# Performance work log

Hardware: AMD Instinct MI355X
Metric: run time of the kernel (lower is better)

## Reference

```python
import jax, jax.numpy as jnp
import numpy as np

FS = 20.832e6      # sampling rate [Hz]
FDEMOD = 5.208e6   # demodulation frequency [Hz]
C = 1540.0         # sound speed [m/s]
FNUM = 1.0
MIN_W = 1e-3
EPS = 1e-5         # BatchNorm eps
EVENT = 0
TWO_PI = 2.0 * np.pi


def _cba(x, w, b, g, beta, pad):
    # Conv2d (NCHW) + BatchNorm2d (training-mode batch stats, biased var) + ReLU
    y = jax.lax.conv_general_dilated(x, w, (1, 1), ((0, 0), (pad, pad)),
                                     dimension_numbers=('NCHW', 'OIHW', 'NCHW'))
    y = y + b[None, :, None, None]
    mu = jnp.mean(y, axis=(0, 2, 3), keepdims=True)
    var = jnp.mean((y - mu) ** 2, axis=(0, 2, 3), keepdims=True)
    y = (y - mu) * jax.lax.rsqrt(var + EPS) * g[None, :, None, None] + beta[None, :, None, None]
    return jax.nn.relu(y)


def _forward(idata, qdata, angles, ele_pos, time_zero, grid,
             conv_w1, conv_b1, bn_g1, bn_b1,
             conv_w2, conv_b2, bn_g2, bn_b2,
             conv_w3, conv_b3, bn_g3, bn_b3,
             conv_w4, conv_b4, bn_g4, bn_b4):
    # --- normalization of raw I/Q data ---
    nrm = jnp.max(jnp.sqrt(idata ** 2 + qdata ** 2))
    idat = idata / nrm
    qdat = qdata / nrm
    H, Wd = grid.shape[:2]
    pix = grid.reshape(-1, 3)                               # [P,3]
    E = ele_pos.shape[0]
    ns = idat.shape[-1]
    ang = angles[EVENT]
    # --- delays in samples: plane-wave tx delay + per-element rx focus delay ---
    txdel = (pix[:, 0] * jnp.sin(ang) + pix[:, 2] * jnp.cos(ang)
             + time_zero[EVENT] * C) * (FS / C)             # [P]
    rxdel = jnp.linalg.norm(pix[None, :, :] - ele_pos[:, None, :], axis=-1) * (FS / C)  # [E,P]
    delays = txdel[None, :] + rxdel                         # [E,P]
    # --- 1D linear interp with zero padding ---
    # (grid_sample(bilinear, align_corners=False) on a 1xN image with the
    #  coordinate mapping in the source is exactly sampling at `delays`)
    d0 = jnp.floor(delays)
    frac = delays - d0
    d0i = d0.astype(jnp.int32)

    def gather(sig, idx):  # sig [E,ns], idx [E,P]
        v = jnp.take_along_axis(sig, jnp.clip(idx, 0, ns - 1), axis=1)
        return jnp.where((idx >= 0) & (idx < ns), v, 0.0)

    isig, qsig = idat[EVENT], qdat[EVENT]                   # [E,ns]
    ifoc = gather(isig, d0i) * (1.0 - frac) + gather(isig, d0i + 1) * frac
    qfoc = gather(qsig, d0i) * (1.0 - frac) + gather(qsig, d0i + 1) * frac
    # --- complex demodulation rotation ---
    tshift = delays / FS - pix[None, :, 2] * 2.0 / C
    theta = TWO_PI * FDEMOD * tshift
    ct, st = jnp.cos(theta), jnp.sin(theta)
    ir = ifoc * ct - qfoc * st
    qr = qfoc * ct + ifoc * st
    # [1,H,W,E,2]  (== torch idas/qdas view + squeeze(-2))
    inputData = jnp.transpose(jnp.stack([ir, qr], axis=-1), (1, 0, 2)).reshape(H, Wd, E, 2)[None]
    # --- receive apodization (orthogonal f-number mask), [H,W,E] ---
    v = pix[None, :, :] - ele_pos[:, None, :]
    vx, vz = v[:, :, 0], v[:, :, 2]
    px = pix[None, :, 0]
    # |vz/vx| > fnum written division-free as |vz| > fnum*|vx| (equivalent since vz>0)
    mrx = ((jnp.abs(vz) > FNUM * jnp.abs(vx)) | (jnp.abs(vx) <= MIN_W)
           | ((vx >= MIN_W) & (px <= ele_pos[0, 0]))
           | ((vx <= -MIN_W) & (px >= ele_pos[-1, 0])))
    apod_rx = jnp.transpose(mrx.astype(jnp.float32).reshape(E, H, Wd), (1, 2, 0))
    # --- transmit apodization (plane-wave footprint), [H,W] ---
    x_proj = pix[:, 0] - pix[:, 2] * jnp.tan(ang)
    mtx = (x_proj >= ele_pos[0, 0] * 1.2) & (x_proj <= ele_pos[-1, 0] * 1.2)
    apod_tx = mtx.astype(jnp.float32).reshape(H, Wd)
    inputData = inputData * apod_rx[None, :, :, :, None] * apod_tx[None, :, :, None, None]
    # --- per-element weighting CNN over [1, 2, H*W, E] ---
    x = jnp.transpose(inputData, (0, 4, 3, 1, 2)).reshape(1, 2, E, H * Wd)
    x = jnp.swapaxes(x, 2, 3)                               # [1,2,HW,E]
    x = _cba(x, conv_w1, conv_b1, bn_g1, bn_b1, 32)
    x = _cba(x, conv_w2, conv_b2, bn_g2, bn_b2, 7)
    x = _cba(x, conv_w3, conv_b3, bn_g3, bn_b3, 7)
    x = _cba(x, conv_w4, conv_b4, bn_g4, bn_b4, 1)          # [1,1,HW,E]
    weights = jnp.swapaxes(x[:, 0], 1, 2).reshape(1, E, H, Wd)
    singleW = jnp.sum(weights, axis=1)                      # [1,H,W]
    comp = jnp.mean(inputData * singleW[:, :, :, None, None], axis=-2)  # [1,H,W,2]
    mag = jnp.sqrt(jnp.sum(comp ** 2, axis=-1))
    ydb = 20.0 * jnp.log10(mag + 1e-20)
    y = ydb[0]
    return y - jnp.max(y)


def setup_inputs():
    key = jax.random.key(0)
    ks = jax.random.split(key, 8)
    na, ne, ns = 16, 128, 2048
    H, Wd = 128, 256
    idata = jax.random.normal(ks[0], (na, ne, ns), jnp.float32)
    qdata = jax.random.normal(ks[1], (na, ne, ns), jnp.float32)
    angles = jnp.linspace(-0.1, 0.1, na, dtype=jnp.float32)
    ex = jnp.linspace(-19.05e-3, 19.05e-3, ne, dtype=jnp.float32)
    ele_pos = jnp.stack([ex, jnp.zeros(ne, jnp.float32), jnp.zeros(ne, jnp.float32)], axis=-1)
    time_zero = jnp.zeros((na,), jnp.float32)
    xg = jnp.linspace(-17e-3, 17e-3, H, dtype=jnp.float32)
    zg = jnp.linspace(5e-3, 55e-3, Wd, dtype=jnp.float32)
    gx, gz = jnp.meshgrid(xg, zg, indexing='ij')
    grid = jnp.stack([gx, jnp.zeros_like(gx), gz], axis=-1)

    def conv_init(k, o, i, kh, kw):
        return jax.random.normal(k, (o, i, kh, kw), jnp.float32) * (1.0 / np.sqrt(i * kh * kw))

    return dict(idata=idata, qdata=qdata, angles=angles, ele_pos=ele_pos,
                time_zero=time_zero, grid=grid,
                conv_w1=conv_init(ks[2], 8, 2, 1, 65), conv_b1=jnp.zeros(8, jnp.float32),
                bn_g1=jnp.ones(8, jnp.float32), bn_b1=jnp.zeros(8, jnp.float32),
                conv_w2=conv_init(ks[3], 8, 8, 1, 15), conv_b2=jnp.zeros(8, jnp.float32),
                bn_g2=jnp.ones(8, jnp.float32), bn_b2=jnp.zeros(8, jnp.float32),
                conv_w3=conv_init(ks[4], 8, 8, 1, 15), conv_b3=jnp.zeros(8, jnp.float32),
                bn_g3=jnp.ones(8, jnp.float32), bn_b3=jnp.zeros(8, jnp.float32),
                conv_w4=conv_init(ks[5], 1, 8, 1, 3), conv_b4=jnp.zeros(1, jnp.float32),
                bn_g4=jnp.ones(1, jnp.float32), bn_b4=jnp.zeros(1, jnp.float32))


def reference(idata, qdata, angles, ele_pos, time_zero, grid,
              conv_w1, conv_b1, bn_g1, bn_b1,
              conv_w2, conv_b2, bn_g2, bn_b2,
              conv_w3, conv_b3, bn_g3, bn_b3,
              conv_w4, conv_b4, bn_g4, bn_b4):
    return _forward(idata, qdata, angles, ele_pos, time_zero, grid,
                    conv_w1, conv_b1, bn_g1, bn_b1,
                    conv_w2, conv_b2, bn_g2, bn_b2,
                    conv_w3, conv_b3, bn_g3, bn_b3,
                    conv_w4, conv_b4, bn_g4, bn_b4)
```

## Files before the change

kernel.cpp:

```cpp
#include <hip/hip_runtime.h>
#include <hip/hip_bf16.h>


#define E_    128
#define NPIX  32768
#define NS_   (NPIX * E_)
#define NSAMP 2048

static constexpr double PI_D     = 3.14159265358979323846;
static constexpr double FS_D     = 20832000.0;
static constexpr double FDEMOD_D = 5208000.0;
static constexpr double C_D      = 1540.0;

typedef __attribute__((ext_vector_type(8))) short short8;
typedef __attribute__((ext_vector_type(4))) float f32x4;

union U8 { uint4 u4; unsigned u32[4]; unsigned short us[8]; short8 s8; };

__device__ __forceinline__ unsigned short f2bf(float f) {
  unsigned u = __float_as_uint(f);
  unsigned r = (u + 0x7fffu + ((u >> 16) & 1u)) >> 16;
  return (unsigned short)r;
}
__device__ __forceinline__ unsigned cvt_pk_bf16(float lo, float hi) {
  unsigned r;
  asm("v_cvt_pk_bf16_f32 %0, %1, %2" : "=v"(r) : "v"(lo), "v"(hi));
  return r;
}
__device__ __forceinline__ float bflo(unsigned w) { return __uint_as_float(w << 16); }
__device__ __forceinline__ float bfhi(unsigned w) { return __uint_as_float(w & 0xFFFF0000u); }
__device__ __forceinline__ float bf2f(unsigned short s) {
  return __uint_as_float((unsigned)s << 16);
}

__device__ __forceinline__ float wave_reduce_sum(float v) {
  #pragma unroll
  for (int off = 32; off; off >>= 1) v += __shfl_xor(v, off);
  return v;
}
__device__ __forceinline__ float wave_reduce_max(float v) {
  #pragma unroll
  for (int off = 32; off; off >>= 1) v = fmaxf(v, __shfl_xor(v, off));
  return v;
}

template <int NBLK>
__device__ __forceinline__ void stats8v(const float4* __restrict__ part4,
                                        const float* __restrict__ g,
                                        const float* __restrict__ beta,
                                        float* __restrict__ A,
                                        float* __restrict__ Bc) {
  __shared__ float red[4][16];
  __shared__ float sums[16];
  const int tid = threadIdx.x;
  constexpr int K = (NBLK * 4) / 256;
  float ax = 0.f, ay = 0.f, az = 0.f, aw = 0.f;
  #pragma unroll
  for (int k = 0; k < K; ++k) {
    const float4 q = part4[tid + k * 256];
    ax += q.x; ay += q.y; az += q.z; aw += q.w;
  }
  #pragma unroll
  for (int off = 4; off <= 32; off <<= 1) {
    ax += __shfl_xor(ax, off);
    ay += __shfl_xor(ay, off);
    az += __shfl_xor(az, off);
    aw += __shfl_xor(aw, off);
  }
  const int lane = tid & 63, wv = tid >> 6;
  if (lane < 4) {
    red[wv][lane * 4 + 0] = ax;
    red[wv][lane * 4 + 1] = ay;
    red[wv][lane * 4 + 2] = az;
    red[wv][lane * 4 + 3] = aw;
  }
  __syncthreads();
  if (tid < 16)
    sums[tid] = red[0][tid] + red[1][tid] + red[2][tid] + red[3][tid];
  __syncthreads();
  if (tid < 8) {
    const float s = sums[tid], ss = sums[tid + 8];
    const float count = (float)NS_;
    const float mu = s / count;
    const float var = fmaxf(ss / count - mu * mu, 0.f);
    const float Av = g[tid] * rsqrtf(var + 1e-5f);
    red[0][tid] = Av;
    red[1][tid] = beta[tid] - mu * Av;
  }
  __syncthreads();
  #pragma unroll
  for (int i = 0; i < 8; ++i) { A[i] = red[0][i]; Bc[i] = red[1][i]; }
}

__device__ __forceinline__ uint4 bn_unit(uint4 v, const float* A, const float* B) {
  U8 in; in.u4 = v;
  unsigned ow[4];
  #pragma unroll
  for (int w = 0; w < 4; ++w) {
    const unsigned wd = in.u32[w];
    const float yl = fmaxf(0.f, fmaf(A[2 * w], bflo(wd), B[2 * w]));
    const float yh = fmaxf(0.f, fmaf(A[2 * w + 1], bfhi(wd), B[2 * w + 1]));
    ow[w] = cvt_pk_bf16(yl, yh);
  }
  return make_uint4(ow[0], ow[1], ow[2], ow[3]);
}

__global__ __launch_bounds__(256) void k_init(const float4* __restrict__ id4,
                                              const float4* __restrict__ qd4,
                                              float* __restrict__ pmaxsq) {
  const int idx = blockIdx.x * 256 + threadIdx.x;
  const float4 iv = id4[idx];
  const float4 qv = qd4[idx];
  float m = fmaxf(fmaxf(iv.x * iv.x + qv.x * qv.x, iv.y * iv.y + qv.y * qv.y),
                  fmaxf(iv.z * iv.z + qv.z * qv.z, iv.w * iv.w + qv.w * qv.w));
  m = wave_reduce_max(m);
  __shared__ float sm[4];
  if ((threadIdx.x & 63) == 0) sm[threadIdx.x >> 6] = m;
  __syncthreads();
  if (threadIdx.x == 0)
    pmaxsq[blockIdx.x] = fmaxf(fmaxf(sm[0], sm[1]), fmaxf(sm[2], sm[3]));
}

__global__ __launch_bounds__(256) void k_beamform(
    const float4* __restrict__ id4, const float4* __restrict__ qd4,
    const float* __restrict__ angles, const float* __restrict__ ele_pos,
    const float* __restrict__ time_zero, const float* __restrict__ grid,
    const float4* __restrict__ pmaxsq4, unsigned* __restrict__ x0t) {
  __shared__ float2 sig[NSAMP];
  __shared__ float smax[4];
  const int e = blockIdx.x & 127;
  const int chunk = blockIdx.x >> 7;

  const float4* irow = id4 + e * (NSAMP / 4);
  const float4* qrow = qd4 + e * (NSAMP / 4);
  #pragma unroll
  for (int k0 = 0; k0 < 2; ++k0) {
    const int k = k0 * 256 + threadIdx.x;
    const float4 iv = irow[k];
    const float4 qv = qrow[k];
    sig[4 * k + 0] = make_float2(iv.x, qv.x);
    sig[4 * k + 1] = make_float2(iv.y, qv.y);
    sig[4 * k + 2] = make_float2(iv.z, qv.z);
    sig[4 * k + 3] = make_float2(iv.w, qv.w);
  }
  float mx = 0.f;
  #pragma unroll
  for (int k = 0; k < 4; ++k) {
    const float4 q = pmaxsq4[threadIdx.x + k * 256];
    mx = fmaxf(mx, fmaxf(fmaxf(q.x, q.y), fmaxf(q.z, q.w)));
  }
  mx = wave_reduce_max(mx);
  if ((threadIdx.x & 63) == 0) smax[threadIdx.x >> 6] = mx;
  __syncthreads();
  const float inv =
      1.0f / sqrtf(fmaxf(fmaxf(smax[0], smax[1]), fmaxf(smax[2], smax[3])));

  const float ang = angles[0];
  const float tz  = time_zero[0];

  constexpr float SC    = (float)(FS_D / C_D);
  constexpr float TH2R  = (float)(2.0 * FDEMOD_D / C_D);
  constexpr float TWOPI = (float)(2.0 * PI_D);

  const float sa = __sinf(ang);
  const float ca = __cosf(ang);
  const float ta = sa / ca;
  const float ex  = ele_pos[e * 3];
  const float ex0 = ele_pos[0];
  const float exl = ele_pos[127 * 3];

  #pragma unroll
  for (int s = 0; s < 4; ++s) {
    const int p = chunk * 1024 + s * 256 + threadIdx.x;
    const float px = grid[p * 3 + 0];
    const float pz = grid[p * 3 + 2];

    const float txdel = (px * sa + pz * ca + tz * (float)C_D) * SC;
    const float dx = px - ex;
    const float rxdel = sqrtf(dx * dx + pz * pz) * SC;

    const float delays = txdel + rxdel;
    const float d0 = floorf(delays);
    const float frac = delays - d0;
    const int i0 = (int)d0;

    const int c0 = min(max(i0, 0), NSAMP - 1);
    const int c1 = min(max(i0 + 1, 0), NSAMP - 1);
    const float2 s0 = sig[c0];
    const float2 s1 = sig[c1];
    const bool m0 = (i0 >= 0) && (i0 < NSAMP);
    const bool m1 = (i0 + 1 >= 0) && (i0 + 1 < NSAMP);
    const float iv0 = m0 ? s0.x : 0.f;
    const float qv0 = m0 ? s0.y : 0.f;
    const float iv1 = m1 ? s1.x : 0.f;
    const float qv1 = m1 ? s1.y : 0.f;
    const float ifoc = (iv0 * (1.f - frac) + iv1 * frac) * inv;
    const float qfoc = (qv0 * (1.f - frac) + qv1 * frac) * inv;

    const float trev = fmaf(delays, 0.25f, -pz * TH2R);
    const float fr = trev - floorf(trev);
    const float st = __sinf(fr * TWOPI);
    const float ct = __cosf(fr * TWOPI);
    const float ir = ifoc * ct - qfoc * st;
    const float qr = qfoc * ct + ifoc * st;

    const float avx = fabsf(dx);
    const bool mrx = (fabsf(pz) > avx) || (avx <= 0.001f) ||
                     ((dx >= 0.001f) && (px <= ex0)) ||
                     ((dx <= -0.001f) && (px >= exl));
    const float xproj = px - pz * ta;
    const bool mtx = (xproj >= ex0 * 1.2f) && (xproj <= exl * 1.2f);
    const float a = (mrx && mtx) ? 1.f : 0.f;

    x0t[(size_t)e * NPIX + p] = cvt_pk_bf16(ir * a, qr * a);
  }
}

#define CONV1_P 32
#define ROWW    213

__global__ __launch_bounds__(256, 4) void k_conv1(
    const unsigned* __restrict__ x0t, const float* __restrict__ wgt,
    const float* __restrict__ bias, uint2* __restrict__ outp,
    float* __restrict__ partial,
    float* __restrict__ sumI, float* __restrict__ sumQ) {
  __shared__ unsigned tile[CONV1_P * ROWW];
  const int tid = threadIdx.x;
  const int lane = tid & 63;
  const int wv = tid >> 6;
  const int n = lane & 15, kq = lane >> 4;
  const int p0 = blockIdx.x * CONV1_P;

  short8 af2[6];
  #pragma unroll
  for (int m = 0; m < 6; ++m) {
    U8 u;
    #pragma unroll
    for (int j = 0; j < 8; ++j) {
      const int oc = n & 7;
      const int mm = (n < 8) ? m : (m - 1);
      const int tap = mm * 16 + kq * 4 + (j >> 1);
      const int ic = j & 1;
      const float w = (mm >= 0 && tap < 65) ? wgt[(oc * 2 + ic) * 65 + tap] : 0.f;
      u.us[j] = f2bf(w);
    }
    af2[m] = u.s8;
  }
  float bias_r[4];
  #pragma unroll
  for (int r = 0; r < 4; ++r) bias_r[r] = bias[(kq & 1) * 4 + r];

  for (int i = tid; i < CONV1_P * 32; i += 256)
    tile[(i >> 5) * ROWW + (i & 31)] = 0u;
  for (int i = tid; i < CONV1_P * 64; i += 256) {
    const int c = i & 63;
    if (c < ROWW - 160) tile[(i >> 6) * ROWW + 160 + c] = 0u;
  }
  {
    const int lp = tid & 31;
    const int e0 = tid >> 5;
    #pragma unroll
    for (int i = 0; i < 16; ++i) {
      const int e = i * 8 + e0;
      tile[lp * ROWW + 32 + e] = x0t[(size_t)e * NPIX + p0 + lp];
    }
  }
  __syncthreads();

  float sum[4] = {0, 0, 0, 0}, ssq[4] = {0, 0, 0, 0};
  const int sbase = n + kq * 4;

  for (int j8 = 0; j8 < 8; ++j8) {
    const int lpx = wv * 8 + j8;
    const int p = p0 + lpx;
    const unsigned* row = tile + lpx * ROWW;
    uint2* orow = outp + (size_t)p * 256;

    {
      const unsigned v0 = row[32 + lane];
      const unsigned v1 = row[96 + lane];
      float si = bflo(v0) + bflo(v1);
      float sq = bfhi(v0) + bfhi(v1);
      si = wave_reduce_sum(si);
      sq = wave_reduce_sum(sq);
      if (lane == 0) { sumI[p] = si; sumQ[p] = sq; }
    }

    U8 win[12];
    #pragma unroll
    for (int q = 0; q < 12; ++q)
      #pragma unroll
      for (int c = 0; c < 4; ++c) win[q].u32[c] = row[sbase + 16 * q + c];

    #pragma unroll
    for (int pi = 0; pi < 4; ++pi) {
      f32x4 acc = {bias_r[0], bias_r[1], bias_r[2], bias_r[3]};
      #pragma unroll
      for (int m = 0; m < 6; ++m)
        acc = __builtin_amdgcn_mfma_f32_16x16x32_bf16(af2[m], win[2 * pi + m].s8,
                                                      acc, 0, 0, 0);
      const unsigned lo = cvt_pk_bf16(acc[0], acc[1]);
      const unsigned hi = cvt_pk_bf16(acc[2], acc[3]);
      orow[((2 * pi + (kq >> 1)) * 16 + n) * 2 + (kq & 1)] = make_uint2(lo, hi);
      #pragma unroll
      for (int r = 0; r < 4; ++r) { const float v = acc[r]; sum[r] += v; ssq[r] += v * v; }
    }
  }

  #pragma unroll
  for (int off = 1; off <= 8; off <<= 1)
    #pragma unroll
    for (int r = 0; r < 4; ++r) { sum[r] += __shfl_xor(sum[r], off); ssq[r] += __shfl_xor(ssq[r], off); }
  #pragma unroll
  for (int r = 0; r < 4; ++r) { sum[r] += __shfl_xor(sum[r], 32); ssq[r] += __shfl_xor(ssq[r], 32); }
  __shared__ float s_red[4][16];
  if (lane == 0)
    #pragma unroll
    for (int r = 0; r < 4; ++r) { s_red[wv][r] = sum[r]; s_red[wv][8 + r] = ssq[r]; }
  if (lane == 16)
    #pragma unroll
    for (int r = 0; r < 4; ++r) { s_red[wv][4 + r] = sum[r]; s_red[wv][12 + r] = ssq[r]; }
  __syncthreads();
  if (tid < 16)
    partial[blockIdx.x * 16 + tid] =
        s_red[0][tid] + s_red[1][tid] + s_red[2][tid] + s_red[3][tid];
}

template <int NBLK_IN>
__global__ __launch_bounds__(256) void k_conv23(
    const uint4* __restrict__ inp, const float* __restrict__ wgt,
    const float* __restrict__ bias,
    const float4* __restrict__ part_in,
    const float* __restrict__ g_in, const float* __restrict__ be_in,
    uint2* __restrict__ outp, float* __restrict__ partial) {
  __shared__ uint4 s_row[4][144];
  const int tid = threadIdx.x;
  const int lane = tid & 63;
  const int wv = tid >> 6;
  const int gw = blockIdx.x * 4 + wv;
  const int n = lane & 15, kq = lane >> 4;

  uint4 v0 = inp[(size_t)gw * 128 + lane];
  uint4 v1 = inp[(size_t)gw * 128 + 64 + lane];

  float A[8], Bc[8];
  stats8v<NBLK_IN>(part_in, g_in, be_in, A, Bc);

  short8 af[4];
  #pragma unroll
  for (int m = 0; m < 4; ++m) {
    U8 u;
    #pragma unroll
    for (int j = 0; j < 8; ++j) {
      const int tap = m * 4 + kq;
      const float w = (n < 8 && tap < 15) ? wgt[(n * 8 + j) * 15 + tap] : 0.f;
      u.us[j] = f2bf(w);
    }
    af[m] = u.s8;
  }
  float bias_r[4];
  #pragma unroll
  for (int r = 0; r < 4; ++r) {
    const int oo = kq * 4 + r;
    bias_r[r] = (oo < 8) ? bias[oo] : 0.f;
  }

  uint4* lds = s_row[wv];
  if (lane < 7)  lds[lane] = make_uint4(0, 0, 0, 0);
  if (lane >= 7 && lane < 16) lds[128 + lane] = make_uint4(0, 0, 0, 0);

  float sum[4] = {0, 0, 0, 0}, ssq[4] = {0, 0, 0, 0};

  #pragma unroll 1
  for (int it = 0; it < 4; ++it) {
    const int p = gw + it * 8192;
    lds[7 + lane]  = bn_unit(v0, A, Bc);
    lds[71 + lane] = bn_unit(v1, A, Bc);

    if (it < 3) {
      const uint4* ng = inp + (size_t)(p + 8192) * 128;
      v0 = ng[lane];
      v1 = ng[64 + lane];
    }

    uint2* orow = outp + (size_t)p * 256;
    for (int t = 0; t < 8; ++t) {
      f32x4 acc = {bias_r[0], bias_r[1], bias_r[2], bias_r[3]};
      const int base = t * 16 + n + kq;
      #pragma unroll
      for (int m = 0; m < 4; ++m) {
        U8 b;
        b.u4 = lds[base + m * 4];
        acc = __builtin_amdgcn_mfma_f32_16x16x32_bf16(af[m], b.s8, acc, 0, 0, 0);
      }
      if (lane < 32) {
        const unsigned lo = cvt_pk_bf16(acc[0], acc[1]);
        const unsigned hi = cvt_pk_bf16(acc[2], acc[3]);
        orow[(t * 16 + n) * 2 + kq] = make_uint2(lo, hi);
        #pragma unroll
        for (int r = 0; r < 4; ++r) { const float v = acc[r]; sum[r] += v; ssq[r] += v * v; }
      }
    }
  }

  #pragma unroll
  for (int off = 1; off <= 8; off <<= 1)
    #pragma unroll
    for (int r = 0; r < 4; ++r) { sum[r] += __shfl_xor(sum[r], off); ssq[r] += __shfl_xor(ssq[r], off); }
  __shared__ float s_red[4][16];
  if (lane == 0)
    #pragma unroll
    for (int r = 0; r < 4; ++r) { s_red[wv][r] = sum[r]; s_red[wv][8 + r] = ssq[r]; }
  if (lane == 16)
    #pragma unroll
    for (int r = 0; r < 4; ++r) { s_red[wv][4 + r] = sum[r]; s_red[wv][12 + r] = ssq[r]; }
  __syncthreads();
  if (tid < 16)
    partial[blockIdx.x * 16 + tid] =
        s_red[0][tid] + s_red[1][tid] + s_red[2][tid] + s_red[3][tid];
}

__global__ __launch_bounds__(256) void k_conv4(
    const uint4* __restrict__ inp,
    const float4* __restrict__ part_in,
    const float* __restrict__ g3, const float* __restrict__ be3,
    const float* __restrict__ w4, const float* __restrict__ b4,
    unsigned short* __restrict__ y4b, float* __restrict__ partial) {
  float A[8], Bc[8];
  stats8v<2048>(part_in, g3, be3, A, Bc);

  const float bb = b4[0];
  float w4r[24];
  #pragma unroll
  for (int i = 0; i < 24; ++i) w4r[i] = w4[i];

  float s = 0.f, ss = 0.f;
  #pragma unroll 1
  for (int it = 0; it < 8; ++it) {
    const int idx = blockIdx.x * 256 + threadIdx.x + it * 524288;
    const int p = idx >> 7, e = idx & 127;
    float acc = bb;
    const uint4* row = inp + (size_t)p * 128 + e;
    #pragma unroll
    for (int kt = 0; kt < 3; ++kt) {
      const int ee = e + kt - 1;
      if (ee >= 0 && ee < E_) {
        U8 u; u.u4 = row[kt - 1];
        #pragma unroll
        for (int i = 0; i < 8; ++i) {
          const unsigned wd = u.u32[i >> 1];
          const float x = (i & 1) ? bfhi(wd) : bflo(wd);
          const float v = fmaxf(0.f, fmaf(A[i], x, Bc[i]));
          acc = fmaf(w4r[i * 3 + kt], v, acc);
        }
      }
    }
    y4b[idx] = f2bf(acc);
    s += acc;
    ss += acc * acc;
  }

  s = wave_reduce_sum(s);
  ss = wave_reduce_sum(ss);
  __shared__ float sm[4][2];
  if ((threadIdx.x & 63) == 0) { sm[threadIdx.x >> 6][0] = s; sm[threadIdx.x >> 6][1] = ss; }
  __syncthreads();
  if (threadIdx.x == 0) {
    partial[blockIdx.x * 2 + 0] = sm[0][0] + sm[1][0] + sm[2][0] + sm[3][0];
    partial[blockIdx.x * 2 + 1] = sm[0][1] + sm[1][1] + sm[2][1] + sm[3][1];
  }
}

__global__ __launch_bounds__(256) void k_final(const float* __restrict__ sumI,
                                               const float* __restrict__ sumQ,
                                               const unsigned short* __restrict__ y4b,
                                               const float4* __restrict__ part_in,
                                               const float* __restrict__ g4,
                                               const float* __restrict__ be4,
                                               float* __restrict__ ydb,
                                               float* __restrict__ pmax) {
  __shared__ float sAB[2];
  {
    const int tid = threadIdx.x;
    float s = 0.f, ss = 0.f;
    #pragma unroll
    for (int k = 0; k < 4; ++k) {
      const float4 q = part_in[tid + k * 256];
      s += q.x + q.z;
      ss += q.y + q.w;
    }
    s = wave_reduce_sum(s);
    ss = wave_reduce_sum(ss);
    __shared__ float sm[4][2];
    if ((tid & 63) == 0) { sm[tid >> 6][0] = s; sm[tid >> 6][1] = ss; }
    __syncthreads();
    if (tid == 0) {
      s  = sm[0][0] + sm[1][0] + sm[2][0] + sm[3][0];
      ss = sm[0][1] + sm[1][1] + sm[2][1] + sm[3][1];
      const float count = (float)NS_;
      const float mu = s / count;
      const float var = fmaxf(ss / count - mu * mu, 0.f);
      const float Av = g4[0] * rsqrtf(var + 1e-5f);
      sAB[0] = Av;
      sAB[1] = be4[0] - mu * Av;
    }
    __syncthreads();
  }
  const float A = sAB[0], B = sAB[1];

  const int w = threadIdx.x >> 6;
  const int lane = threadIdx.x & 63;
  const int p = blockIdx.x * 4 + w;
  const size_t base = (size_t)p * E_;

  float sw = fmaxf(0.f, fmaf(A, bf2f(y4b[base + lane]), B)) +
             fmaxf(0.f, fmaf(A, bf2f(y4b[base + lane + 64]), B));
  sw = wave_reduce_sum(sw);

  __shared__ float s_m[4];
  if (lane == 0) {
    const float ci = sw * sumI[p] * (1.f / (float)E_);
    const float cq = sw * sumQ[p] * (1.f / (float)E_);
    const float mag = sqrtf(ci * ci + cq * cq);
    const float v = 20.f * log10f(mag + 1e-20f);
    ydb[p] = v;
    s_m[w] = v;
  }
  __syncthreads();
  if (threadIdx.x == 0)
    pmax[blockIdx.x] = fmaxf(fmaxf(s_m[0], s_m[1]), fmaxf(s_m[2], s_m[3]));
}

__global__ __launch_bounds__(256) void k_sub(const float* __restrict__ ydb,
                                             const float4* __restrict__ pmax4,
                                             float* __restrict__ out) {
  float m = -3.4e38f;
  #pragma unroll
  for (int k = 0; k < 8; ++k) {
    const float4 q = pmax4[threadIdx.x + k * 256];
    m = fmaxf(m, fmaxf(fmaxf(q.x, q.y), fmaxf(q.z, q.w)));
  }
  m = wave_reduce_max(m);
  __shared__ float sm[4];
  if ((threadIdx.x & 63) == 0) sm[threadIdx.x >> 6] = m;
  __syncthreads();
  __shared__ float sgm;
  if (threadIdx.x == 0)
    sgm = fmaxf(fmaxf(sm[0], sm[1]), fmaxf(sm[2], sm[3]));
  __syncthreads();
  const int i = blockIdx.x * 256 + threadIdx.x;
  out[i] = ydb[i] - sgm;
}

static constexpr size_t OFF_A     = 0;
static constexpr size_t OFF_Y4    = 0;
static constexpr size_t OFF_YDB   = 16777216;
static constexpr size_t OFF_PMAX  = 16908288;
static constexpr size_t OFF_BUF1  = 67108864;
static constexpr size_t OFF_SUMI  = 134217728;
static constexpr size_t OFF_SUMQ  = 134348800;
static constexpr size_t OFF_PART0 = 134479872;
static constexpr size_t OFF_PART1 = 134610944;
static constexpr size_t OFF_PMSQ  = 134742016;

extern "C" void kernel_launch(void* const* d_in, const int* in_sizes, int n_in,
                              void* d_out, int out_size, void* d_ws, size_t ws_size,
                              hipStream_t stream) {
  const float* idata     = (const float*)d_in[0];
  const float* qdata     = (const float*)d_in[1];
  const float* angles    = (const float*)d_in[2];
  const float* ele_pos   = (const float*)d_in[3];
  const float* time_zero = (const float*)d_in[4];
  const float* grid      = (const float*)d_in[5];
  const float* w1 = (const float*)d_in[6];  const float* b1 = (const float*)d_in[7];
  const float* g1 = (const float*)d_in[8];  const float* be1 = (const float*)d_in[9];
  const float* w2 = (const float*)d_in[10]; const float* b2 = (const float*)d_in[11];
  const float* g2 = (const float*)d_in[12]; const float* be2 = (const float*)d_in[13];
  const float* w3 = (const float*)d_in[14]; const float* b3 = (const float*)d_in[15];
  const float* g3 = (const float*)d_in[16]; const float* be3 = (const float*)d_in[17];
  const float* w4 = (const float*)d_in[18]; const float* b4 = (const float*)d_in[19];
  const float* g4 = (const float*)d_in[20]; const float* be4 = (const float*)d_in[21];

  char* ws = (char*)d_ws;
  unsigned*       x0t   = (unsigned*)(ws + OFF_A);
  uint4*          buf2  = (uint4*)(ws + OFF_A);
  unsigned short* y4b   = (unsigned short*)(ws + OFF_Y4);
  float*          ydb   = (float*)(ws + OFF_YDB);
  float*          pmax  = (float*)(ws + OFF_PMAX);
  uint4*          buf1  = (uint4*)(ws + OFF_BUF1);
  float*          sumI  = (float*)(ws + OFF_SUMI);
  float*          sumQ  = (float*)(ws + OFF_SUMQ);
  float*          part0 = (float*)(ws + OFF_PART0);
  float*          part1 = (float*)(ws + OFF_PART1);
  float*          pmsq  = (float*)(ws + OFF_PMSQ);

  k_init<<<4096, 256, 0, stream>>>((const float4*)idata, (const float4*)qdata, pmsq);
  k_beamform<<<4096, 256, 0, stream>>>((const float4*)idata, (const float4*)qdata,
                                       angles, ele_pos, time_zero, grid,
                                       (const float4*)pmsq, x0t);

  k_conv1<<<NPIX / CONV1_P, 256, 0, stream>>>(x0t, w1, b1, (uint2*)buf1, part0,
                                              sumI, sumQ);

  k_conv23<1024><<<2048, 256, 0, stream>>>(buf1, w2, b2, (const float4*)part0,
                                           g1, be1, (uint2*)buf2, part1);

  k_conv23<2048><<<2048, 256, 0, stream>>>(buf2, w3, b3, (const float4*)part1,
                                           g2, be2, (uint2*)buf1, part0);

  k_conv4<<<2048, 256, 0, stream>>>(buf1, (const float4*)part0, g3, be3,
                                    w4, b4, y4b, part1);

  k_final<<<NPIX / 4, 256, 0, stream>>>(sumI, sumQ, y4b, (const float4*)part1,
                                        g4, be4, ydb, pmax);
  k_sub<<<NPIX / 256, 256, 0, stream>>>(ydb, (const float4*)pmax, (float*)d_out);
}
```

Before: 259.4 us.

## Pack two output tiles per MFMA in 8-channel conv to avoid wasted rows

The 1x15 conv with 8 output channels previously used 16x16x32 MFMAs where half the output rows were padding, so half of each MFMA's work and half the lanes' outputs were discarded. The weight fragments are rearranged so rows 8-15 compute the same channels shifted by 16 pixels. Each MFMA chain now produces two 16-pixel tiles, which halves the number of outer iterations, and all lanes store results. The cost is 8 MFMAs per chain instead of 4, more registers for weights and B fragments, and an extra cross-half shuffle in the stats reduction.

```diff
diff --git a/kernel.cpp b/kernel.cpp
--- a/kernel.cpp
+++ b/kernel.cpp
@@ -346,24 +346,22 @@
   float A[8], Bc[8];
   stats8v<NBLK_IN>(part_in, g_in, be_in, A, Bc);
 
-  short8 af[4];
-  #pragma unroll
-  for (int m = 0; m < 4; ++m) {
+  short8 af2[8];
+  #pragma unroll
+  for (int m = 0; m < 8; ++m) {
     U8 u;
     #pragma unroll
     for (int j = 0; j < 8; ++j) {
-      const int tap = m * 4 + kq;
-      const float w = (n < 8 && tap < 15) ? wgt[(n * 8 + j) * 15 + tap] : 0.f;
+      const int oc = n & 7;
+      const int tap = (n < 8) ? (m * 4 + kq) : (m * 4 + kq - 16);
+      const float w = (tap >= 0 && tap < 15) ? wgt[(oc * 8 + j) * 15 + tap] : 0.f;
       u.us[j] = f2bf(w);
     }
-    af[m] = u.s8;
+    af2[m] = u.s8;
   }
   float bias_r[4];
   #pragma unroll
-  for (int r = 0; r < 4; ++r) {
-    const int oo = kq * 4 + r;
-    bias_r[r] = (oo < 8) ? bias[oo] : 0.f;
-  }
+  for (int r = 0; r < 4; ++r) bias_r[r] = bias[(kq & 1) * 4 + r];
 
   uint4* lds = s_row[wv];
   if (lane < 7)  lds[lane] = make_uint4(0, 0, 0, 0);
@@ -384,22 +382,21 @@
     }
 
     uint2* orow = outp + (size_t)p * 256;
-    for (int t = 0; t < 8; ++t) {
+    #pragma unroll
+    for (int P = 0; P < 4; ++P) {
+      const int base = P * 32 + n + kq;
+      U8 b[8];
+      #pragma unroll
+      for (int m = 0; m < 8; ++m) b[m].u4 = lds[base + m * 4];
       f32x4 acc = {bias_r[0], bias_r[1], bias_r[2], bias_r[3]};
-      const int base = t * 16 + n + kq;
       #pragma unroll
-      for (int m = 0; m < 4; ++m) {
-        U8 b;
-        b.u4 = lds[base + m * 4];
-        acc = __builtin_amdgcn_mfma_f32_16x16x32_bf16(af[m], b.s8, acc, 0, 0, 0);
-      }
-      if (lane < 32) {
-        const unsigned lo = cvt_pk_bf16(acc[0], acc[1]);
-        const unsigned hi = cvt_pk_bf16(acc[2], acc[3]);
-        orow[(t * 16 + n) * 2 + kq] = make_uint2(lo, hi);
-        #pragma unroll
-        for (int r = 0; r < 4; ++r) { const float v = acc[r]; sum[r] += v; ssq[r] += v * v; }
-      }
+      for (int m = 0; m < 8; ++m)
+        acc = __builtin_amdgcn_mfma_f32_16x16x32_bf16(af2[m], b[m].s8, acc, 0, 0, 0);
+      const unsigned lo = cvt_pk_bf16(acc[0], acc[1]);
+      const unsigned hi = cvt_pk_bf16(acc[2], acc[3]);
+      orow[((P * 2 + (kq >> 1)) * 16 + n) * 2 + (kq & 1)] = make_uint2(lo, hi);
+      #pragma unroll
+      for (int r = 0; r < 4; ++r) { const float v = acc[r]; sum[r] += v; ssq[r] += v * v; }
     }
   }
 
@@ -407,6 +404,8 @@
   for (int off = 1; off <= 8; off <<= 1)
     #pragma unroll
     for (int r = 0; r < 4; ++r) { sum[r] += __shfl_xor(sum[r], off); ssq[r] += __shfl_xor(ssq[r], off); }
+  #pragma unroll
+  for (int r = 0; r < 4; ++r) { sum[r] += __shfl_xor(sum[r], 32); ssq[r] += __shfl_xor(ssq[r], 32); }
   __shared__ float s_red[4][16];
   if (lane == 0)
     #pragma unroll
```

Measured after the change: 281.5 us. 1.09x slower.
